# Kernel tuning notes

Measured on AMD Instinct MI355X. Metric: run time of the kernel, lower is better.

## Reference

```python
import jax, jax.numpy as jnp
import numpy as np

N, C, T, V = 64, 64, 256, 25
S, OC = 3, 64
IC = OC // 2  # inter_channels
BN_EPS = 1e-5


def setup_inputs() -> dict:
    key = jax.random.key(0)
    ks = jax.random.split(key, 8)
    return {
        "x": jax.random.normal(ks[0], (N, C, T, V), dtype=jnp.float32),
        "A": jax.random.normal(ks[1], (S, V, V), dtype=jnp.float32),
        "Wa": jax.random.normal(ks[2], (S, IC, C), dtype=jnp.float32) * 0.05,
        "ba": jax.random.normal(ks[3], (S, IC), dtype=jnp.float32) * 0.05,
        "Wb": jax.random.normal(ks[4], (S, IC, C), dtype=jnp.float32) * 0.05,
        "bb": jax.random.normal(ks[5], (S, IC), dtype=jnp.float32) * 0.05,
        "Wd": jax.random.normal(ks[6], (S, OC, C), dtype=jnp.float32) * 0.05,
        "bd": jax.random.normal(ks[7], (S, OC), dtype=jnp.float32) * 0.05,
        "bn_gamma": jnp.ones((OC,), dtype=jnp.float32),
        "bn_beta": jnp.zeros((OC,), dtype=jnp.float32),
    }


def reference(x, A, Wa, ba, Wb, bb, Wd, bd, bn_gamma, bn_beta):
    n, c, t, v = x.shape
    s, ic = Wa.shape[0], Wa.shape[1]
    # 1x1 convs over all subsets at once: [N,S,IC,T,V]
    a = jnp.einsum('nctv,sic->nsitv', x, Wa) + ba[None, :, :, None, None]
    b = jnp.einsum('nctv,sic->nsitv', x, Wb) + bb[None, :, :, None, None]
    # A1: permute(0,3,1,2).view(N,V,IC*T) per subset -> [N,S,V,IC*T]
    A1 = a.transpose(0, 1, 4, 2, 3).reshape(n, s, v, ic * t)
    # A2: view(N,IC*T,V) per subset -> [N,S,IC*T,V]
    A2 = b.reshape(n, s, ic * t, v)
    scores = jnp.einsum('nsvk,nskw->nsvw', A1, A2) / (ic * t)
    # torch Softmax(-2): normalize over the first V axis (rows of [V,V])
    att = jax.nn.softmax(scores, axis=-2) + A[None]  # [N,S,V,V]
    # x.view(N,C*T,V) @ att  ->  contract over source joint v
    z = jnp.einsum('nctv,nsvw->nsctw', x, att)  # [N,S,C,T,V]
    # conv_d per subset then sum over subsets (the y accumulation)
    y = jnp.einsum('nsctw,soc->notw', z, Wd) + bd.sum(0)[None, :, None, None]
    # BatchNorm2d in inference mode with running_mean=0, running_var=1
    y = bn_gamma[None, :, None, None] * y * (1.0 / jnp.sqrt(1.0 + BN_EPS)) + bn_beta[None, :, None, None]
    # residual=False -> residual(x) == 0; self.relu is defined but never applied
    return y
```

## Files before the change

### kernel.cpp

```cpp
#include <hip/hip_runtime.h>


#define NCHUNK    16
#define ATT_OFF   0
#define ATT_SZ    (64*3*25*32)
#define PART_OFF  153600
#define PART_SZ   (64*NCHUNK*3*625)
#define WAT_OFF   (PART_OFF + PART_SZ)
#define WBT_OFF   (WAT_OFF + 3*64*32)
#define WDT_OFF   (WBT_OFF + 3*64*32)
#define ALPHA_OFF (WDT_OFF + 3*64*64)
#define BETA_OFF  (ALPHA_OFF + 64)

__global__ __launch_bounds__(256) void k0_prep(
    float* __restrict__ wsf,
    const float* __restrict__ Wa, const float* __restrict__ Wb,
    const float* __restrict__ Wd, const float* __restrict__ bd,
    const float* __restrict__ gamma, const float* __restrict__ beta)
{
  int idx = blockIdx.x * 256 + threadIdx.x;
  if (idx < 6144) {
    int s = idx / 2048, r = idx - s * 2048, c = r >> 5, i = r & 31;
    wsf[WAT_OFF + idx] = Wa[s * 2048 + i * 64 + c];
    wsf[WBT_OFF + idx] = Wb[s * 2048 + i * 64 + c];
  }
  if (idx < 12288) {
    int s = idx / 4096, r = idx - s * 4096, c = r >> 6, o = r & 63;
    wsf[WDT_OFF + idx] = Wd[s * 4096 + o * 64 + c];
  }
  if (idx < 64) {
    float al = gamma[idx] * rsqrtf(1.0f + 1e-5f);
    wsf[ALPHA_OFF + idx] = al;
    float bs = bd[idx] + bd[64 + idx] + bd[128 + idx];
    wsf[BETA_OFF + idx] = beta[idx] + al * bs;
  }
}

__global__ __launch_bounds__(256) void k1_scores(
    const float* __restrict__ x,
    const float* __restrict__ WaT, const float* __restrict__ WbT,
    const float* __restrict__ ba, const float* __restrict__ bb,
    float* __restrict__ part)
{
  const int nb = blockIdx.x;
  const int n = nb >> 4;
  const int ch = nb & 15;
  const int tid = threadIdx.x;
  const int wave = tid >> 6;
  const int lane = tid & 63;
  const int tgrp = wave >> 1;
  const int i0 = __builtin_amdgcn_readfirstlane((wave & 1) << 4);
  const int tl = tgrp * 2 + lane / 25;
  const int tlc = tl < 4 ? tl : 3;
  const int v = lane % 25;
  const bool act = lane < 50;
  const int tlv = tgrp * 50 + lane;

  __shared__ float ab[6400];
  __shared__ float red[1875];
  float* const red2 = ab;

  const int tp = tid % 25;
  const int ks = tid / 25;
  const int v5 = (tp / 5) * 5, w5 = (tp % 5) * 5;
  const int kb = (ks < 8) ? ks * 13 : (104 + (ks - 8) * 12);
  const int kcnt = (ks < 8) ? 13 : 12;

  for (int idx = tid; idx < 1875; idx += 256) red[idx] = 0.0f;
  __syncthreads();

  for (int sub = 0; sub < 4; ++sub) {
    const int t0 = ch * 16 + sub * 4;
    for (int s = 0; s < 3; ++s) {
      float fa[16], fb[16];
      #pragma unroll
      for (int j = 0; j < 16; ++j) {
        fa[j] = ba[s * 32 + i0 + j];
        fb[j] = bb[s * 32 + i0 + j];
      }
      const float* xp = x + n * 409600 + (t0 + tlc) * 25 + v;
      const float* wap = WaT + s * 2048 + i0;
      const float* wbp = WbT + s * 2048 + i0;
      for (int c8 = 0; c8 < 64; c8 += 8) {
        float xv[8];
        #pragma unroll
        for (int u = 0; u < 8; ++u)
          xv[u] = act ? xp[(c8 + u) * 6400] : 0.0f;
        #pragma unroll
        for (int u = 0; u < 8; ++u) {
          const float* wa8 = wap + (c8 + u) * 32;
          const float* wb8 = wbp + (c8 + u) * 32;
          #pragma unroll
          for (int j = 0; j < 16; ++j) {
            fa[j] = fmaf(wa8[j], xv[u], fa[j]);
            fb[j] = fmaf(wb8[j], xv[u], fb[j]);
          }
        }
      }
      __syncthreads();
      if (act) {
        #pragma unroll
        for (int j = 0; j < 16; ++j) {
          ab[(i0 + j) * 100 + tlv]        = fa[j];
          ab[3200 + (i0 + j) * 100 + tlv] = fb[j];
        }
      }
      __syncthreads();
      float sc[5][5];
      if (tid < 250) {
        #pragma unroll
        for (int dv = 0; dv < 5; ++dv)
          #pragma unroll
          for (int dw = 0; dw < 5; ++dw) sc[dv][dw] = 0.0f;
        for (int kk = 0; kk < kcnt; ++kk) {
          const int k = kb + kk;
          float av[5], bv[5];
          #pragma unroll
          for (int d = 0; d < 5; ++d) {
            av[d] = ab[k * 25 + v5 + d];
            bv[d] = ab[3200 + k * 25 + w5 + d];
          }
          #pragma unroll
          for (int dv = 0; dv < 5; ++dv)
            #pragma unroll
            for (int dw = 0; dw < 5; ++dw)
              sc[dv][dw] = fmaf(av[dv], bv[dw], sc[dv][dw]);
        }
      }
      __syncthreads();
      if (tid < 250) {
        #pragma unroll
        for (int dv = 0; dv < 5; ++dv)
          #pragma unroll
          for (int dw = 0; dw < 5; ++dw)
            red2[ks * 625 + (v5 + dv) * 25 + (w5 + dw)] = sc[dv][dw];
      }
      __syncthreads();
      {
        float acc0 = 0.0f, acc1 = 0.0f, acc2 = 0.0f;
        #pragma unroll
        for (int q = 0; q < 10; ++q) {
          acc0 += red2[q * 625 + tid];
          acc1 += red2[q * 625 + tid + 256];
          if (tid < 113) acc2 += red2[q * 625 + tid + 512];
        }
        red[s * 625 + tid]        += acc0;
        red[s * 625 + tid + 256]  += acc1;
        if (tid < 113) red[s * 625 + tid + 512] += acc2;
      }
    }
  }
  __syncthreads();
  for (int s = 0; s < 3; ++s)
    for (int idx = tid; idx < 625; idx += 256)
      part[((n * NCHUNK + ch) * 3 + s) * 625 + idx] = red[s * 625 + idx];
}

__global__ __launch_bounds__(64) void k2_softmax(
    const float* __restrict__ part, const float* __restrict__ A,
    float* __restrict__ att)
{
  const int ns = blockIdx.x;
  const int n = ns / 3, s = ns % 3;
  const int w = threadIdx.x;
  float* ap = att + ns * 800;
  if (w < 25) {
    float sc[25];
    float m = -3.0e38f;
    #pragma unroll
    for (int v = 0; v < 25; ++v) {
      float acc = 0.0f;
      for (int chk = 0; chk < NCHUNK; ++chk)
        acc += part[((n * NCHUNK + chk) * 3 + s) * 625 + v * 25 + w];
      sc[v] = acc * (1.0f / 8192.0f);
      m = fmaxf(m, sc[v]);
    }
    float sum = 0.0f;
    #pragma unroll
    for (int v = 0; v < 25; ++v) { sc[v] = expf(sc[v] - m); sum += sc[v]; }
    const float inv = 1.0f / sum;
    #pragma unroll
    for (int v = 0; v < 25; ++v)
      ap[v * 32 + w] = sc[v] * inv + A[(s * 25 + v) * 25 + w];
  } else if (w < 32) {
    for (int v = 0; v < 25; ++v) ap[v * 32 + w] = 0.0f;
  }
}

__global__ __launch_bounds__(256) void k3_out(
    const float* __restrict__ x, const float* __restrict__ att,
    const float* __restrict__ WdT,
    const float* __restrict__ alpha, const float* __restrict__ betaE,
    float* __restrict__ out)
{
  const int nb = blockIdx.x;
  const int n = nb >> 7;
  const int t0 = (nb & 127) * 2;
  const int tid = threadIdx.x;
  const int wave = tid >> 6;
  const int lane = tid & 63;

  __shared__ float xs[3200];
  __shared__ float zt[4224];

  const float* xg = x + n * 409600 + t0 * 25;
  for (int idx = tid; idx < 3200; idx += 256) {
    int c = idx / 50, p = idx - c * 50;
    xs[idx] = xg[c * 6400 + p];
  }

  const int c0A = __builtin_amdgcn_readfirstlane((wave & 1) << 5);
  const int w0A = __builtin_amdgcn_readfirstlane((wave >> 1) << 4);
  const int o0B = __builtin_amdgcn_readfirstlane(wave << 4);
  const int tB = lane >> 5, wB = lane & 31;
  const int xbase = c0A * 50 + lane * 25;
  const int zwb   = c0A * 66 + lane * 33 + w0A;
  const int zrb   = tB * 33 + wB;

  float yacc[16];
  #pragma unroll
  for (int j = 0; j < 16; ++j) yacc[j] = 0.0f;

  __syncthreads();
  for (int s = 0; s < 3; ++s) {
    const float* attp = att + (n * 3 + s) * 800 + w0A;
    float za[16];
    #pragma unroll
    for (int j = 0; j < 16; ++j) za[j] = 0.0f;
    #pragma unroll 5
    for (int v = 0; v < 25; ++v) {
      float xv = xs[xbase + v];
      #pragma unroll
      for (int j = 0; j < 16; ++j)
        za[j] = fmaf(attp[v * 32 + j], xv, za[j]);
    }
    #pragma unroll
    for (int j = 0; j < 16; ++j) zt[zwb + j] = za[j];
    __syncthreads();
    const float* wdp = WdT + s * 4096 + o0B;
    #pragma unroll 4
    for (int c = 0; c < 64; ++c) {
      float zv = zt[c * 66 + zrb];
      #pragma unroll
      for (int j = 0; j < 16; ++j)
        yacc[j] = fmaf(wdp[c * 64 + j], zv, yacc[j]);
    }
    __syncthreads();
  }
  if (wB < 25) {
    const int t = t0 + tB;
    float* op = out + n * 409600 + t * 25 + wB;
    #pragma unroll
    for (int j = 0; j < 16; ++j) {
      const int o = o0B + j;
      op[o * 6400] = alpha[o] * yacc[j] + betaE[o];
    }
  }
}

extern "C" void kernel_launch(void* const* d_in, const int* in_sizes, int n_in,
                              void* d_out, int out_size, void* d_ws, size_t ws_size,
                              hipStream_t stream) {
  const float* x     = (const float*)d_in[0];
  const float* A     = (const float*)d_in[1];
  const float* Wa    = (const float*)d_in[2];
  const float* ba    = (const float*)d_in[3];
  const float* Wb    = (const float*)d_in[4];
  const float* bb    = (const float*)d_in[5];
  const float* Wd    = (const float*)d_in[6];
  const float* bd    = (const float*)d_in[7];
  const float* gamma = (const float*)d_in[8];
  const float* beta  = (const float*)d_in[9];
  float* wsf = (float*)d_ws;
  float* out = (float*)d_out;

  k0_prep<<<64, 256, 0, stream>>>(wsf, Wa, Wb, Wd, bd, gamma, beta);
  k1_scores<<<1024, 256, 0, stream>>>(x, wsf + WAT_OFF, wsf + WBT_OFF,
                                      ba, bb, wsf + PART_OFF);
  k2_softmax<<<192, 64, 0, stream>>>(wsf + PART_OFF, A, wsf + ATT_OFF);
  k3_out<<<8192, 256, 0, stream>>>(x, wsf + ATT_OFF, wsf + WDT_OFF,
                                   wsf + ALPHA_OFF, wsf + BETA_OFF, out);
}
```

Before: 571.2 us.

## Hoist x loads into registers across subsets, pad LDS tiles, parallelize softmax reduction

In k1_scores, the 64 x values per thread are loaded once per time sub-chunk and reused across all three subsets instead of being reloaded for each subset. The LDS a/b tiles are padded to a 28-float stride, and launch bounds request 3 waves per EU. k2_softmax now reduces the partial scores with 256 threads into shared memory before the per-column softmax. k3_out caches its 25 x values in registers across subsets. The extra live registers risk spills or lower occupancy.

```diff
diff --git a/kernel.cpp b/kernel.cpp
--- a/kernel.cpp
+++ b/kernel.cpp
@@ -36,7 +36,7 @@
   }
 }
 
-__global__ __launch_bounds__(256) void k1_scores(
+__global__ __launch_bounds__(256, 3) void k1_scores(
     const float* __restrict__ x,
     const float* __restrict__ WaT, const float* __restrict__ WbT,
     const float* __restrict__ ba, const float* __restrict__ bb,
@@ -54,9 +54,8 @@
   const int tlc = tl < 4 ? tl : 3;
   const int v = lane % 25;
   const bool act = lane < 50;
-  const int tlv = tgrp * 50 + lane;
-
-  __shared__ float ab[6400];
+
+  __shared__ float ab[7168];
   __shared__ float red[1875];
   float* const red2 = ab;
 
@@ -69,8 +68,16 @@
   for (int idx = tid; idx < 1875; idx += 256) red[idx] = 0.0f;
   __syncthreads();
 
+  #pragma unroll 1
   for (int sub = 0; sub < 4; ++sub) {
     const int t0 = ch * 16 + sub * 4;
+    const float* xp = x + n * 409600 + (t0 + tlc) * 25 + v;
+    float xv[64];
+    #pragma unroll
+    for (int c = 0; c < 64; ++c)
+      xv[c] = act ? xp[c * 6400] : 0.0f;
+
+    #pragma unroll 1
     for (int s = 0; s < 3; ++s) {
       float fa[16], fb[16];
       #pragma unroll
@@ -78,31 +85,22 @@
         fa[j] = ba[s * 32 + i0 + j];
         fb[j] = bb[s * 32 + i0 + j];
       }
-      const float* xp = x + n * 409600 + (t0 + tlc) * 25 + v;
       const float* wap = WaT + s * 2048 + i0;
       const float* wbp = WbT + s * 2048 + i0;
-      for (int c8 = 0; c8 < 64; c8 += 8) {
-        float xv[8];
-        #pragma unroll
-        for (int u = 0; u < 8; ++u)
-          xv[u] = act ? xp[(c8 + u) * 6400] : 0.0f;
-        #pragma unroll
-        for (int u = 0; u < 8; ++u) {
-          const float* wa8 = wap + (c8 + u) * 32;
-          const float* wb8 = wbp + (c8 + u) * 32;
-          #pragma unroll
-          for (int j = 0; j < 16; ++j) {
-            fa[j] = fmaf(wa8[j], xv[u], fa[j]);
-            fb[j] = fmaf(wb8[j], xv[u], fb[j]);
-          }
+      #pragma unroll
+      for (int c = 0; c < 64; ++c) {
+        #pragma unroll
+        for (int j = 0; j < 16; ++j) {
+          fa[j] = fmaf(wap[c * 32 + j], xv[c], fa[j]);
+          fb[j] = fmaf(wbp[c * 32 + j], xv[c], fb[j]);
         }
       }
       __syncthreads();
       if (act) {
         #pragma unroll
         for (int j = 0; j < 16; ++j) {
-          ab[(i0 + j) * 100 + tlv]        = fa[j];
-          ab[3200 + (i0 + j) * 100 + tlv] = fb[j];
+          ab[(i0 + j) * 112 + tl * 28 + v]        = fa[j];
+          ab[3584 + (i0 + j) * 112 + tl * 28 + v] = fb[j];
         }
       }
       __syncthreads();
@@ -117,8 +115,8 @@
           float av[5], bv[5];
           #pragma unroll
           for (int d = 0; d < 5; ++d) {
-            av[d] = ab[k * 25 + v5 + d];
-            bv[d] = ab[3200 + k * 25 + w5 + d];
+            av[d] = ab[k * 28 + v5 + d];
+            bv[d] = ab[3584 + k * 28 + w5 + d];
           }
           #pragma unroll
           for (int dv = 0; dv < 5; ++dv)
@@ -156,32 +154,35 @@
       part[((n * NCHUNK + ch) * 3 + s) * 625 + idx] = red[s * 625 + idx];
 }
 
-__global__ __launch_bounds__(64) void k2_softmax(
+__global__ __launch_bounds__(256) void k2_softmax(
     const float* __restrict__ part, const float* __restrict__ A,
     float* __restrict__ att)
 {
   const int ns = blockIdx.x;
   const int n = ns / 3, s = ns % 3;
-  const int w = threadIdx.x;
+  const int tid = threadIdx.x;
+  __shared__ float sm[625];
+  for (int idx = tid; idx < 625; idx += 256) {
+    float acc = 0.0f;
+    #pragma unroll
+    for (int chk = 0; chk < NCHUNK; ++chk)
+      acc += part[((n * NCHUNK + chk) * 3 + s) * 625 + idx];
+    sm[idx] = acc * (1.0f / 8192.0f);
+  }
+  __syncthreads();
   float* ap = att + ns * 800;
+  const int w = tid;
   if (w < 25) {
-    float sc[25];
     float m = -3.0e38f;
     #pragma unroll
-    for (int v = 0; v < 25; ++v) {
-      float acc = 0.0f;
-      for (int chk = 0; chk < NCHUNK; ++chk)
-        acc += part[((n * NCHUNK + chk) * 3 + s) * 625 + v * 25 + w];
-      sc[v] = acc * (1.0f / 8192.0f);
-      m = fmaxf(m, sc[v]);
-    }
-    float sum = 0.0f;
-    #pragma unroll
-    for (int v = 0; v < 25; ++v) { sc[v] = expf(sc[v] - m); sum += sc[v]; }
+    for (int v = 0; v < 25; ++v) m = fmaxf(m, sm[v * 25 + w]);
+    float e[25], sum = 0.0f;
+    #pragma unroll
+    for (int v = 0; v < 25; ++v) { e[v] = expf(sm[v * 25 + w] - m); sum += e[v]; }
     const float inv = 1.0f / sum;
     #pragma unroll
     for (int v = 0; v < 25; ++v)
-      ap[v * 32 + w] = sc[v] * inv + A[(s * 25 + v) * 25 + w];
+      ap[v * 32 + w] = e[v] * inv + A[(s * 25 + v) * 25 + w];
   } else if (w < 32) {
     for (int v = 0; v < 25; ++v) ap[v * 32 + w] = 0.0f;
   }
@@ -222,17 +223,21 @@
   for (int j = 0; j < 16; ++j) yacc[j] = 0.0f;
 
   __syncthreads();
+  float xreg[25];
+  #pragma unroll
+  for (int v = 0; v < 25; ++v) xreg[v] = xs[xbase + v];
+
+  #pragma unroll 1
   for (int s = 0; s < 3; ++s) {
     const float* attp = att + (n * 3 + s) * 800 + w0A;
     float za[16];
     #pragma unroll
     for (int j = 0; j < 16; ++j) za[j] = 0.0f;
-    #pragma unroll 5
+    #pragma unroll
     for (int v = 0; v < 25; ++v) {
-      float xv = xs[xbase + v];
       #pragma unroll
       for (int j = 0; j < 16; ++j)
-        za[j] = fmaf(attp[v * 32 + j], xv, za[j]);
+        za[j] = fmaf(attp[v * 32 + j], xreg[v], za[j]);
     }
     #pragma unroll
     for (int j = 0; j < 16; ++j) zt[zwb + j] = za[j];
@@ -277,7 +282,7 @@
   k0_prep<<<64, 256, 0, stream>>>(wsf, Wa, Wb, Wd, bd, gamma, beta);
   k1_scores<<<1024, 256, 0, stream>>>(x, wsf + WAT_OFF, wsf + WBT_OFF,
                                       ba, bb, wsf + PART_OFF);
-  k2_softmax<<<192, 64, 0, stream>>>(wsf + PART_OFF, A, wsf + ATT_OFF);
+  k2_softmax<<<192, 256, 0, stream>>>(wsf + PART_OFF, A, wsf + ATT_OFF);
   k3_out<<<8192, 256, 0, stream>>>(x, wsf + ATT_OFF, wsf + WDT_OFF,
                                    wsf + ALPHA_OFF, wsf + BETA_OFF, out);
 }
```

Result: slower. 704.3 us (+23.3%).
